# Performance work log

Measured on AMD Instinct MI355X. Metric: run time of the kernel, lower is better.

Reference implementation:

```python
import jax, jax.numpy as jnp
import numpy as np

N = 256      # max_num_nodes (padded nodes per graph)
H = 8        # attention heads
F = 128      # feature_dim
L = 9        # n_layers
INFLA = 6.0  # MCL inflation
EPS = 1e-6


def _layernorm(x, g, b):
    mu = x.mean(-1, keepdims=True)
    var = ((x - mu) ** 2).mean(-1, keepdims=True)
    return (x - mu) / jnp.sqrt(var + 1e-5) * g + b


def _get_mcl(adj):
    # Markov-cluster style power iteration with inflation every 3rd step (num=6)
    m = adj / (adj.sum(-1, keepdims=True) + EPS)
    r = m
    for i in range(6):
        r = m @ r
        if (i + 1) % 3 == 0:
            r = r ** INFLA
        r = r / (r.sum(-1, keepdims=True) + EPS)
    return r


def _forward(input_x, edge_attr, gcn_lin_w, gcn_root_emb, gcn_edge_w,
             gcn_norm_g, gcn_norm_b, ln_in_g, ln_in_b, ln_ffn_g, ln_ffn_b,
             mcl_w, q_w, k_w, v_w, merge_w, merge_b,
             ffn_w1, ffn_b1, ffn_w2, ffn_b2, final_g, final_b,
             edge_index, n_counts, root):
    BN = input_x.shape[0]
    B = BN // N
    dh = F // H
    row, col = edge_index[0], edge_index[1]

    # --- adjacency / padding masks (built once, as in GC_T.forward) ---
    valid = jnp.arange(N)[None, :] < n_counts[:, None]                    # [B,N]
    eb, es, et = row // N, row % N, col % N
    adj = jnp.zeros((B, N, N), bool).at[eb, es, et].set(True)
    adj = adj | (jnp.eye(N, dtype=bool)[None] & valid[:, :, None])        # self loops on valid nodes
    pad = ~(valid[:, :, None] & valid[:, None, :])
    pad_bias = jnp.where(pad, -1024.0, 0.0)[..., None]                    # [B,N,N,1] (broadcast over H)
    mcl = _get_mcl(adj.astype(input_x.dtype))[..., None]                  # [B,N,N,1]

    # --- GCN degree normalization (degree of row index, +1) ---
    deg = jnp.zeros((BN,), input_x.dtype).at[row].add(1.0) + 1.0
    dis = deg ** -0.5
    enorm = (dis[row] * dis[col])[:, None]                                # [E,1]

    out = input_x.reshape(B, N, F)
    for i in range(L):
        # ---- GCNConv: gather-relu-scatter message passing ----
        res = out
        h = out.reshape(BN, F) @ gcn_lin_w[i].T                           # [BN,F]
        ee = edge_attr @ gcn_edge_w[i].T                                  # [E,F]
        msg = enorm * jax.nn.relu(h[row] + ee)                            # x_j = x[row]
        agg = jax.ops.segment_sum(msg, col, num_segments=BN)              # aggregate at target
        g = agg + jax.nn.relu(h + gcn_root_emb[i][root]) / deg[:, None]
        g = jax.nn.relu(_layernorm(g, gcn_norm_g[i], gcn_norm_b[i]))
        out = g.reshape(B, N, F) + res

        # ---- Encoder: biased multi-head attention + FFN ----
        bias4 = (pad_bias + mcl * mcl_w[i][:, 0]).transpose(0, 3, 1, 2)   # [B,H,N,N]
        x = out
        q = (x @ q_w[i].T).reshape(B, N, H, dh).transpose(0, 2, 1, 3) * (dh ** -0.5)
        k = (x @ k_w[i].T).reshape(B, N, H, dh).transpose(0, 2, 1, 3)
        v = (x @ v_w[i].T).reshape(B, N, H, dh).transpose(0, 2, 1, 3)
        att = jax.nn.softmax(jnp.einsum('bhnd,bhmd->bhnm', q, k) + bias4, axis=-1)
        o = jnp.einsum('bhnm,bhmd->bhnd', att, v).transpose(0, 2, 1, 3).reshape(B, N, F)
        o = o @ merge_w[i].T + merge_b[i]
        x = _layernorm(o + x, ln_in_g[i], ln_in_b[i])
        f = jax.nn.gelu(x @ ffn_w1[i].T + ffn_b1[i], approximate=False)
        f = f @ ffn_w2[i].T + ffn_b2[i]
        out = _layernorm(x + f, ln_ffn_g[i], ln_ffn_b[i])

    return _layernorm(out, final_g, final_b)


def setup_inputs() -> dict:
    key = jax.random.key(0)
    ks = jax.random.split(key, 16)
    B, E = 16, 65536
    s = 0.02 * L ** -0.5
    w = lambda k, shape: jax.random.normal(k, shape, jnp.float32) * s
    return {
        'input_x': jax.random.normal(ks[0], (B * N, F), jnp.float32),
        'edge_attr': jax.random.normal(ks[1], (E, 7), jnp.float32),
        'gcn_lin_w': w(ks[2], (L, F, F)),
        'gcn_root_emb': jax.random.normal(ks[3], (L, 2, F), jnp.float32) * 0.02,
        'gcn_edge_w': w(ks[4], (L, F, 7)),
        'gcn_norm_g': jnp.ones((L, F), jnp.float32),
        'gcn_norm_b': jnp.zeros((L, F), jnp.float32),
        'ln_in_g': jnp.ones((L, F), jnp.float32),
        'ln_in_b': jnp.zeros((L, F), jnp.float32),
        'ln_ffn_g': jnp.ones((L, F), jnp.float32),
        'ln_ffn_b': jnp.zeros((L, F), jnp.float32),
        'mcl_w': w(ks[5], (L, H, 1)),
        'q_w': w(ks[6], (L, F, F)),
        'k_w': w(ks[7], (L, F, F)),
        'v_w': w(ks[8], (L, F, F)),
        'merge_w': w(ks[9], (L, F, F)),
        'merge_b': jnp.zeros((L, F), jnp.float32),
        'ffn_w1': w(ks[10], (L, 2 * F, F)),
        'ffn_b1': jnp.zeros((L, 2 * F), jnp.float32),
        'ffn_w2': w(ks[11], (L, F, 2 * F)),
        'ffn_b2': jnp.zeros((L, F), jnp.float32),
        'final_g': jnp.ones((F,), jnp.float32),
        'final_b': jnp.zeros((F,), jnp.float32),
        'edge_index': jax.random.randint(ks[12], (2, E), 0, B * N),
        'n_counts': jax.random.randint(ks[13], (B,), 1, N + 1),
        'root': jax.random.randint(ks[14], (B * N,), 0, 2),
    }


def reference(input_x, edge_attr, gcn_lin_w, gcn_root_emb, gcn_edge_w,
              gcn_norm_g, gcn_norm_b, ln_in_g, ln_in_b, ln_ffn_g, ln_ffn_b,
              mcl_w, q_w, k_w, v_w, merge_w, merge_b,
              ffn_w1, ffn_b1, ffn_w2, ffn_b2, final_g, final_b,
              edge_index, n_counts, root):
    return _forward(input_x, edge_attr, gcn_lin_w, gcn_root_emb, gcn_edge_w,
                    gcn_norm_g, gcn_norm_b, ln_in_g, ln_in_b, ln_ffn_g, ln_ffn_b,
                    mcl_w, q_w, k_w, v_w, merge_w, merge_b,
                    ffn_w1, ffn_b1, ffn_w2, ffn_b2, final_g, final_b,
                    edge_index, n_counts, root)
```

## Files before the change

kernel.cpp:

```cpp
#include <hip/hip_runtime.h>
#include <hip/hip_bf16.h>
#include <math.h>

#define NLAYER 9

typedef unsigned short u16;
typedef __attribute__((ext_vector_type(8))) short short8;
typedef __attribute__((ext_vector_type(4))) float f32x4;

__device__ inline u16 f2bf(float x) {
  unsigned int u = __float_as_uint(x);
  unsigned int r = (u + 0x7fffu + ((u >> 16) & 1u)) >> 16;
  return (u16)r;
}
__device__ inline float gelu_exact(float x) {
  return 0.5f * x * (1.0f + erff(x * 0.7071067811865476f));
}

__global__ void setup1_kernel(const int* __restrict__ ei, float* __restrict__ adj,
                              float* __restrict__ deg, int* __restrict__ ccount, int E, int EB,
                              const float* __restrict__ s0, const float* __restrict__ s1,
                              const float* __restrict__ s2, const float* __restrict__ s3,
                              const float* __restrict__ s4, const float* __restrict__ s5,
                              const float* __restrict__ s6, u16* __restrict__ d0,
                              u16* __restrict__ d1, u16* __restrict__ d2,
                              u16* __restrict__ d3, u16* __restrict__ d4,
                              u16* __restrict__ d5, u16* __restrict__ d6) {
  int bid = blockIdx.x;
  if (bid < EB) {
    int e = bid * 256 + threadIdx.x;
    if (e >= E) return;
    int r = ei[e], c = ei[E + e];
    int b = r >> 8;
    adj[((size_t)b << 16) + ((size_t)(r & 255) << 8) + (c & 255)] = 1.0f;
    atomicAdd(&deg[r], 1.0f);
    atomicAdd(&ccount[c], 1);
  } else {
    int idx = bid - EB;
    int f = idx / 72, cb = idx % 72;
    const float* s;
    u16* d;
    int n;
    switch (f) {
      case 0: s = s0; d = d0; n = NLAYER * 4096; break;
      case 1: s = s1; d = d1; n = NLAYER * 4096; break;
      case 2: s = s2; d = d2; n = NLAYER * 4096; break;
      case 3: s = s3; d = d3; n = NLAYER * 4096; break;
      case 4: s = s4; d = d4; n = NLAYER * 4096; break;
      case 5: s = s5; d = d5; n = NLAYER * 8192; break;
      default: s = s6; d = d6; n = NLAYER * 8192; break;
    }
    for (int i = cb * 256 + threadIdx.x; i < n; i += 72 * 256) {
      float4 v = ((const float4*)s)[i];
      u16 p4[4] = {f2bf(v.x), f2bf(v.y), f2bf(v.z), f2bf(v.w)};
      ((ushort4*)d)[i] = *(ushort4*)p4;
    }
  }
}

__global__ __launch_bounds__(1024) void setup2_kernel(const int* __restrict__ nc,
                                                      float* __restrict__ adj,
                                                      float* __restrict__ deg,
                                                      float* __restrict__ dis,
                                                      const int* __restrict__ ccount,
                                                      int* __restrict__ rowptr, int BN) {
  int bid = blockIdx.x;
  int t = threadIdx.x;
  if (bid < (BN >> 10)) {
    int n = bid * 1024 + t;
    int b = n >> 8, i = n & 255;
    if (i < nc[b]) adj[((size_t)b << 16) + ((size_t)i << 8) + i] = 1.0f;
    float d = deg[n] + 1.0f;
    deg[n] = d;
    dis[n] = rsqrtf(d);
  } else {
    __shared__ int part[1024];
    int base = t * 4;
    int c[4], s = 0;
#pragma unroll
    for (int i = 0; i < 4; i++) { c[i] = (base + i < BN) ? ccount[base + i] : 0; s += c[i]; }
    part[t] = s;
    __syncthreads();
    for (int o = 1; o < 1024; o <<= 1) {
      int v = (t >= o) ? part[t - o] : 0;
      __syncthreads();
      part[t] += v;
      __syncthreads();
    }
    int excl = part[t] - s;
#pragma unroll
    for (int i = 0; i < 4; i++) {
      if (base + i < BN) rowptr[base + i] = excl;
      excl += c[i];
    }
    if (t == 1023) rowptr[BN] = part[1023];
  }
}

__global__ __launch_bounds__(256) void setup3_kernel(const float* __restrict__ m,
                                                     float* __restrict__ rsinv,
                                                     const int* __restrict__ ei,
                                                     const float* __restrict__ dis,
                                                     const int* __restrict__ rowptr,
                                                     int* __restrict__ fill,
                                                     int* __restrict__ src_s,
                                                     int* __restrict__ eidx_s,
                                                     float* __restrict__ enorm_s, int E,
                                                     int BN) {
  int bid = blockIdx.x;
  int w = threadIdx.x >> 6, lane = threadIdx.x & 63;
  if (bid < (BN >> 2)) {
    int row = bid * 4 + w;
    float4 v4 = *(const float4*)(m + (size_t)row * 256 + lane * 4);
    float s = v4.x + v4.y + v4.z + v4.w;
#pragma unroll
    for (int o = 32; o > 0; o >>= 1) s += __shfl_xor(s, o, 64);
    if (lane == 0) rsinv[row] = 1.f / (s + 1e-6f);
  } else {
    int e = (bid - (BN >> 2)) * 256 + threadIdx.x;
    if (e >= E) return;
    int r = ei[e], c = ei[E + e];
    int pos = rowptr[c] + atomicAdd(&fill[c], 1);
    src_s[pos] = r;
    eidx_s[pos] = e;
    enorm_s[pos] = dis[r] * dis[c];
  }
}

__global__ __launch_bounds__(256) void mcl_prep_kernel(const float* __restrict__ m,
                                                       const float* __restrict__ rsinv,
                                                       u16* __restrict__ mb,
                                                       u16* __restrict__ rT) {
  int b = blockIdx.z;
  const float* M = m + ((size_t)b << 16);
  u16* MB = mb + ((size_t)b << 16);
  u16* RT = rT + ((size_t)b << 16);
  int r0 = blockIdx.x * 64, c0 = blockIdx.y * 64;
  __shared__ float ts[64][65];
  int t = threadIdx.x;
  int i = t >> 2, jb = (t & 3) * 16;
  float riv = rsinv[(b << 8) + r0 + i];
#pragma unroll
  for (int g = 0; g < 4; g++) {
    int j = jb + g * 4;
    float4 v = *(const float4*)(M + (size_t)(r0 + i) * 256 + c0 + j);
    v.x *= riv; v.y *= riv; v.z *= riv; v.w *= riv;
    ts[i][j] = v.x; ts[i][j + 1] = v.y; ts[i][j + 2] = v.z; ts[i][j + 3] = v.w;
    u16 p4[4] = {f2bf(v.x), f2bf(v.y), f2bf(v.z), f2bf(v.w)};
    *(ushort4*)(MB + (size_t)(r0 + i) * 256 + c0 + j) = *(ushort4*)p4;
  }
  __syncthreads();
#pragma unroll
  for (int g = 0; g < 4; g++) {
    int j = jb + g * 4;
    u16 p4[4] = {f2bf(ts[j][i]), f2bf(ts[j + 1][i]), f2bf(ts[j + 2][i]), f2bf(ts[j + 3][i])};
    *(ushort4*)(RT + (size_t)(c0 + i) * 256 + r0 + j) = *(ushort4*)p4;
  }
}

__global__ __launch_bounds__(256) void mcl_iter_kernel(const u16* __restrict__ rT,
                                                       const u16* __restrict__ mb,
                                                       u16* __restrict__ rTn,
                                                       float* __restrict__ mclr,
                                                       int inflate, int fin) {
  __shared__ float red[64];
  int b = blockIdx.x >> 4, i0 = (blockIdx.x & 15) * 16;
  int w = threadIdx.x >> 6, lane = threadIdx.x & 63;
  int m16 = lane & 15, quad = lane >> 4;
  const u16* A = rT + ((size_t)b << 16);
  const u16* Bm = mb + ((size_t)b << 16);
  f32x4 acc[4];
#pragma unroll
  for (int tj = 0; tj < 4; tj++) acc[tj] = (f32x4){0.f, 0.f, 0.f, 0.f};
  for (int k0 = 0; k0 < 256; k0 += 32) {
    short8 bb = *(const short8*)(Bm + (size_t)(i0 + m16) * 256 + k0 + quad * 8);
#pragma unroll
    for (int tj = 0; tj < 4; tj++) {
      short8 a = *(const short8*)(A + (size_t)(w * 64 + tj * 16 + m16) * 256 + k0 + quad * 8);
      acc[tj] = __builtin_amdgcn_mfma_f32_16x16x32_bf16(a, bb, acc[tj], 0, 0, 0);
    }
  }
  float ps = 0.f;
#pragma unroll
  for (int tj = 0; tj < 4; tj++)
#pragma unroll
    for (int reg = 0; reg < 4; reg++) {
      float v = acc[tj][reg];
      if (inflate) { float v2 = v * v; v = v2 * v2 * v2; }
      acc[tj][reg] = v;
      ps += v;
    }
  ps += __shfl_xor(ps, 16, 64);
  ps += __shfl_xor(ps, 32, 64);
  if (quad == 0) red[w * 16 + m16] = ps;
  __syncthreads();
  float tot = red[m16] + red[16 + m16] + red[32 + m16] + red[48 + m16];
  float inv = 1.f / (tot + 1e-6f);
  if (fin) {
    float* dst = mclr + ((size_t)b << 16);
#pragma unroll
    for (int tj = 0; tj < 4; tj++)
#pragma unroll
      for (int reg = 0; reg < 4; reg++) {
        int j = w * 64 + tj * 16 + quad * 4 + reg;
        dst[(size_t)(i0 + m16) * 256 + j] = acc[tj][reg] * inv;
      }
  } else {
    u16* dst = rTn + ((size_t)b << 16);
#pragma unroll
    for (int tj = 0; tj < 4; tj++)
#pragma unroll
      for (int reg = 0; reg < 4; reg++) {
        int j = w * 64 + tj * 16 + quad * 4 + reg;
        dst[(size_t)j * 256 + i0 + m16] = f2bf(acc[tj][reg] * inv);
      }
  }
}

__global__ __launch_bounds__(256) void copyx_lin_kernel(const float* __restrict__ x,
                                                        const u16* __restrict__ wlin0,
                                                        float* __restrict__ outb,
                                                        float* __restrict__ hbuf) {
  __shared__ u16 st[16 * 136];
  int m0 = blockIdx.x * 16;
  int tid = threadIdx.x;
  int w = tid >> 6, lane = tid & 63;
  int m16 = lane & 15, quad = lane >> 4;
  for (int i = tid; i < 2048; i += 256) {
    int row = i >> 7, col = i & 127;
    float v = x[(size_t)(m0 + row) * 128 + col];
    outb[(size_t)(m0 + row) * 128 + col] = v;
    st[row * 136 + col] = f2bf(v);
  }
  __syncthreads();
  int c0 = w * 32;
  f32x4 acc[2] = {{0.f, 0.f, 0.f, 0.f}, {0.f, 0.f, 0.f, 0.f}};
#pragma unroll
  for (int k0 = 0; k0 < 128; k0 += 32) {
    short8 a = *(const short8*)(st + m16 * 136 + k0 + quad * 8);
#pragma unroll
    for (int t = 0; t < 2; t++) {
      short8 bb = *(const short8*)(wlin0 + (size_t)(c0 + t * 16 + m16) * 128 + k0 + quad * 8);
      acc[t] = __builtin_amdgcn_mfma_f32_16x16x32_bf16(a, bb, acc[t], 0, 0, 0);
    }
  }
#pragma unroll
  for (int t = 0; t < 2; t++)
#pragma unroll
    for (int reg = 0; reg < 4; reg++)
      hbuf[(size_t)(m0 + quad * 4 + reg) * 128 + c0 + t * 16 + m16] = acc[t][reg];
}

__global__ __launch_bounds__(256) void gcn_ln_kernel(
    const int* __restrict__ rowptr, const int* __restrict__ src_s,
    const int* __restrict__ eidx_s, const float* __restrict__ enorm_s,
    const float* __restrict__ ea, const float* __restrict__ We, const float* __restrict__ h,
    const float* __restrict__ remb, const int* __restrict__ root,
    const float* __restrict__ deg, const float* __restrict__ gamma,
    const float* __restrict__ beta, float* __restrict__ out, u16* __restrict__ out16) {
  __shared__ float Wt[7 * 128];
  __shared__ float part[2][2][128];
  for (int idx = threadIdx.x; idx < 896; idx += 256) {
    int f = idx & 127, k = idx >> 7;
    Wt[k * 128 + f] = We[f * 7 + k];
  }
  __syncthreads();
  int w = threadIdx.x >> 6, lane = threadIdx.x & 63;
  int nodeSlot = w >> 1, wv = w & 1;
  int n = blockIdx.x * 2 + nodeSlot;
  int f0 = lane, f1 = lane + 64;
  int p0 = rowptr[n], p1 = rowptr[n + 1];
  float a0 = 0.f, a1 = 0.f;
  int p = p0 + wv;
  int r = 0, e = 0;
  float en = 0.f, h0 = 0.f, h1 = 0.f;
  if (p < p1) {
    r = src_s[p];
    e = eidx_s[p];
    en = enorm_s[p];
    h0 = h[(size_t)r * 128 + f0];
    h1 = h[(size_t)r * 128 + f1];
  }
  for (; p < p1; p += 2) {
    int enx = 0;
    float ennx = 0.f, hn0 = 0.f, hn1 = 0.f;
    if (p + 2 < p1) {
      int rn = src_s[p + 2];
      enx = eidx_s[p + 2];
      ennx = enorm_s[p + 2];
      hn0 = h[(size_t)rn * 128 + f0];
      hn1 = h[(size_t)rn * 128 + f1];
    }
    const float* eae = ea + (size_t)e * 7;
    float d0 = 0.f, d1 = 0.f;
#pragma unroll
    for (int k = 0; k < 7; k++) {
      float ev = eae[k];
      d0 += ev * Wt[k * 128 + f0];
      d1 += ev * Wt[k * 128 + f1];
    }
    a0 += en * fmaxf(h0 + d0, 0.f);
    a1 += en * fmaxf(h1 + d1, 0.f);
    e = enx;
    en = ennx;
    h0 = hn0;
    h1 = hn1;
  }
  part[nodeSlot][wv][lane] = a0;
  part[nodeSlot][wv][64 + lane] = a1;
  __syncthreads();
  if (wv == 0) {
    a0 = part[nodeSlot][0][lane] + part[nodeSlot][1][lane];
    a1 = part[nodeSlot][0][64 + lane] + part[nodeSlot][1][64 + lane];
    float invd = 1.0f / deg[n];
    const float* re = remb + root[n] * 128;
    size_t base = (size_t)n * 128;
    float g0 = a0 + fmaxf(h[base + f0] + re[f0], 0.f) * invd;
    float g1 = a1 + fmaxf(h[base + f1] + re[f1], 0.f) * invd;
    float s = g0 + g1, ss = g0 * g0 + g1 * g1;
#pragma unroll
    for (int o = 32; o > 0; o >>= 1) {
      s += __shfl_xor(s, o, 64);
      ss += __shfl_xor(ss, o, 64);
    }
    float mu = s * 0.0078125f;
    float var = ss * 0.0078125f - mu * mu;
    float rs = rsqrtf(var + 1e-5f);
    float y0 = fmaxf((g0 - mu) * rs * gamma[f0] + beta[f0], 0.f) + out[base + f0];
    float y1 = fmaxf((g1 - mu) * rs * gamma[f1] + beta[f1], 0.f) + out[base + f1];
    out[base + f0] = y0;
    out[base + f1] = y1;
    out16[base + f0] = f2bf(y0);
    out16[base + f1] = f2bf(y1);
  }
}

__global__ __launch_bounds__(256) void attn_qkv_kernel(
    const u16* __restrict__ x16, const u16* __restrict__ wq, const u16* __restrict__ wk,
    const u16* __restrict__ wv, const float* __restrict__ mclr,
    const float* __restrict__ mclw, const int* __restrict__ ncnt, u16* __restrict__ o) {
  __shared__ float ks[256][16];
  __shared__ float vs[256][16];
  __shared__ float qs[64][16];
  int qt = blockIdx.x, hh = blockIdx.y, b = blockIdx.z;
  int t = threadIdx.x;
  int w = t >> 6, lane = t & 63;
  int m16 = lane & 15, quad = lane >> 4;
  const u16* bk = wk + (size_t)(hh * 16 + m16) * 128 + quad * 8;
  const u16* bv = wv + (size_t)(hh * 16 + m16) * 128 + quad * 8;
#pragma unroll
  for (int tj = 0; tj < 4; tj++) {
    int rb = w * 64 + tj * 16;
    const u16* arow = x16 + (size_t)(b * 256 + rb + m16) * 128 + quad * 8;
    f32x4 ak = {0.f, 0.f, 0.f, 0.f}, av = {0.f, 0.f, 0.f, 0.f};
#pragma unroll
    for (int k0 = 0; k0 < 128; k0 += 32) {
      short8 a = *(const short8*)(arow + k0);
      ak = __builtin_amdgcn_mfma_f32_16x16x32_bf16(a, *(const short8*)(bk + k0), ak, 0, 0, 0);
      av = __builtin_amdgcn_mfma_f32_16x16x32_bf16(a, *(const short8*)(bv + k0), av, 0, 0, 0);
    }
#pragma unroll
    for (int reg = 0; reg < 4; reg++) {
      ks[rb + quad * 4 + reg][m16] = ak[reg];
      vs[rb + quad * 4 + reg][m16] = av[reg];
    }
  }
  {
    const u16* bq = wq + (size_t)(hh * 16 + m16) * 128 + quad * 8;
    const u16* arow = x16 + (size_t)(b * 256 + qt * 64 + w * 16 + m16) * 128 + quad * 8;
    f32x4 aq = {0.f, 0.f, 0.f, 0.f};
#pragma unroll
    for (int k0 = 0; k0 < 128; k0 += 32) {
      short8 a = *(const short8*)(arow + k0);
      aq = __builtin_amdgcn_mfma_f32_16x16x32_bf16(a, *(const short8*)(bq + k0), aq, 0, 0, 0);
    }
#pragma unroll
    for (int reg = 0; reg < 4; reg++) qs[w * 16 + quad * 4 + reg][m16] = aq[reg] * 0.25f;
  }
  __syncthreads();
  int i = qt * 64 + (t >> 2);
  int d0 = (t & 3) * 4;
  int nc = ncnt[b];
  bool vi = i < nc;
  float wh = mclw[hh];
  float qv[4] = {qs[t >> 2][d0], qs[t >> 2][d0 + 1], qs[t >> 2][d0 + 2], qs[t >> 2][d0 + 3]};
  const float* mrow = mclr + ((size_t)(b * 256 + i)) * 256;
  float acc[4] = {0.f, 0.f, 0.f, 0.f};
  float lsum = 0.f;
  for (int j0 = 0; j0 < 256; j0 += 4) {
    float4 mc = *(const float4*)(mrow + j0);
    float mcv[4] = {mc.x, mc.y, mc.z, mc.w};
#pragma unroll
    for (int jj = 0; jj < 4; jj++) {
      int j = j0 + jj;
      float s = qv[0] * ks[j][d0] + qv[1] * ks[j][d0 + 1] + qv[2] * ks[j][d0 + 2] +
                qv[3] * ks[j][d0 + 3];
      s += __shfl_xor(s, 1, 64);
      s += __shfl_xor(s, 2, 64);
      float bias = mcv[jj] * wh + ((vi && j >= nc) ? -1024.f : 0.f);
      float pe = __expf(s + bias);
      lsum += pe;
      acc[0] += pe * vs[j][d0];
      acc[1] += pe * vs[j][d0 + 1];
      acc[2] += pe * vs[j][d0 + 2];
      acc[3] += pe * vs[j][d0 + 3];
    }
  }
  float inv = 1.f / lsum;
  u16 p4[4] = {f2bf(acc[0] * inv), f2bf(acc[1] * inv), f2bf(acc[2] * inv), f2bf(acc[3] * inv)};
  *(ushort4*)(o + ((size_t)(b * 256 + i) * 128 + hh * 16 + d0)) = *(ushort4*)p4;
}

__global__ __launch_bounds__(256) void merge_ffn_kernel(
    const u16* __restrict__ ob16, const u16* __restrict__ Wm, const float* __restrict__ mb,
    const float* __restrict__ gam1, const float* __restrict__ bet1,
    const u16* __restrict__ W1, const float* __restrict__ b1, const u16* __restrict__ W2,
    const float* __restrict__ b2, const float* __restrict__ gam2,
    const float* __restrict__ bet2, float* __restrict__ outb,
    const u16* __restrict__ wlin_next, float* __restrict__ hbuf,
    const float* __restrict__ fing, const float* __restrict__ finb) {
  __shared__ float redS[64], redSS[64];
  __shared__ u16 st[16 * 136];
  __shared__ u16 f1s[16 * 264];
  int tid = threadIdx.x;
  int w = tid >> 6, lane = tid & 63;
  int m16 = lane & 15, quad = lane >> 4;
  int m0 = blockIdx.x * 16;
  f32x4 acc[2] = {{0.f, 0.f, 0.f, 0.f}, {0.f, 0.f, 0.f, 0.f}};
  {
    const u16* arow = ob16 + (size_t)(m0 + m16) * 128 + quad * 8;
#pragma unroll
    for (int k0 = 0; k0 < 128; k0 += 32) {
      short8 a = *(const short8*)(arow + k0);
#pragma unroll
      for (int t = 0; t < 2; t++) {
        short8 bb = *(const short8*)(Wm + (size_t)(w * 32 + t * 16 + m16) * 128 + k0 + quad * 8);
        acc[t] = __builtin_amdgcn_mfma_f32_16x16x32_bf16(a, bb, acc[t], 0, 0, 0);
      }
    }
  }
  float s4[4] = {0.f, 0.f, 0.f, 0.f}, ss4[4] = {0.f, 0.f, 0.f, 0.f};
#pragma unroll
  for (int t = 0; t < 2; t++) {
    int col = w * 32 + t * 16 + m16;
    float bi = mb[col];
#pragma unroll
    for (int reg = 0; reg < 4; reg++) {
      int row = m0 + quad * 4 + reg;
      float v = acc[t][reg] + bi + outb[(size_t)row * 128 + col];
      acc[t][reg] = v;
      s4[reg] += v;
      ss4[reg] += v * v;
    }
  }
#pragma unroll
  for (int o = 1; o <= 8; o <<= 1)
#pragma unroll
    for (int reg = 0; reg < 4; reg++) {
      s4[reg] += __shfl_xor(s4[reg], o, 64);
      ss4[reg] += __shfl_xor(ss4[reg], o, 64);
    }
  if (m16 == 0) {
#pragma unroll
    for (int reg = 0; reg < 4; reg++) {
      redS[w * 16 + quad * 4 + reg] = s4[reg];
      redSS[w * 16 + quad * 4 + reg] = ss4[reg];
    }
  }
  __syncthreads();
  float mu[4], rsd[4];
#pragma unroll
  for (int reg = 0; reg < 4; reg++) {
    int r = quad * 4 + reg;
    float S = redS[r] + redS[16 + r] + redS[32 + r] + redS[48 + r];
    float SS = redSS[r] + redSS[16 + r] + redSS[32 + r] + redSS[48 + r];
    mu[reg] = S * 0.0078125f;
    float var = SS * 0.0078125f - mu[reg] * mu[reg];
    rsd[reg] = rsqrtf(var + 1e-5f);
  }
  float xr[2][4];
#pragma unroll
  for (int t = 0; t < 2; t++) {
    int col = w * 32 + t * 16 + m16;
    float g = gam1[col], be = bet1[col];
#pragma unroll
    for (int reg = 0; reg < 4; reg++) {
      float y = (acc[t][reg] - mu[reg]) * rsd[reg] * g + be;
      xr[t][reg] = y;
      st[(quad * 4 + reg) * 136 + col] = f2bf(y);
    }
  }
  __syncthreads();
  {
    f32x4 acc1[4];
#pragma unroll
    for (int t = 0; t < 4; t++) acc1[t] = (f32x4){0.f, 0.f, 0.f, 0.f};
#pragma unroll
    for (int k0 = 0; k0 < 128; k0 += 32) {
      short8 a = *(const short8*)(st + m16 * 136 + k0 + quad * 8);
#pragma unroll
      for (int t = 0; t < 4; t++) {
        short8 bb = *(const short8*)(W1 + (size_t)(w * 64 + t * 16 + m16) * 128 + k0 + quad * 8);
        acc1[t] = __builtin_amdgcn_mfma_f32_16x16x32_bf16(a, bb, acc1[t], 0, 0, 0);
      }
    }
#pragma unroll
    for (int t = 0; t < 4; t++) {
      int col = w * 64 + t * 16 + m16;
      float bi = b1[col];
#pragma unroll
      for (int reg = 0; reg < 4; reg++)
        f1s[(quad * 4 + reg) * 264 + col] = f2bf(gelu_exact(acc1[t][reg] + bi));
    }
  }
  __syncthreads();
#pragma unroll
  for (int t = 0; t < 2; t++) acc[t] = (f32x4){0.f, 0.f, 0.f, 0.f};
#pragma unroll
  for (int k0 = 0; k0 < 256; k0 += 32) {
    short8 a = *(const short8*)(f1s + m16 * 264 + k0 + quad * 8);
#pragma unroll
    for (int t = 0; t < 2; t++) {
      short8 bb = *(const short8*)(W2 + (size_t)(w * 32 + t * 16 + m16) * 256 + k0 + quad * 8);
      acc[t] = __builtin_amdgcn_mfma_f32_16x16x32_bf16(a, bb, acc[t], 0, 0, 0);
    }
  }
#pragma unroll
  for (int reg = 0; reg < 4; reg++) { s4[reg] = 0.f; ss4[reg] = 0.f; }
#pragma unroll
  for (int t = 0; t < 2; t++) {
    int col = w * 32 + t * 16 + m16;
    float bi = b2[col];
#pragma unroll
    for (int reg = 0; reg < 4; reg++) {
      float v = acc[t][reg] + bi + xr[t][reg];
      acc[t][reg] = v;
      s4[reg] += v;
      ss4[reg] += v * v;
    }
  }
#pragma unroll
  for (int o = 1; o <= 8; o <<= 1)
#pragma unroll
    for (int reg = 0; reg < 4; reg++) {
      s4[reg] += __shfl_xor(s4[reg], o, 64);
      ss4[reg] += __shfl_xor(ss4[reg], o, 64);
    }
  __syncthreads();
  if (m16 == 0) {
#pragma unroll
    for (int reg = 0; reg < 4; reg++) {
      redS[w * 16 + quad * 4 + reg] = s4[reg];
      redSS[w * 16 + quad * 4 + reg] = ss4[reg];
    }
  }
  __syncthreads();
#pragma unroll
  for (int reg = 0; reg < 4; reg++) {
    int r = quad * 4 + reg;
    float S = redS[r] + redS[16 + r] + redS[32 + r] + redS[48 + r];
    float SS = redSS[r] + redSS[16 + r] + redSS[32 + r] + redSS[48 + r];
    mu[reg] = S * 0.0078125f;
    float var = SS * 0.0078125f - mu[reg] * mu[reg];
    rsd[reg] = rsqrtf(var + 1e-5f);
  }
#pragma unroll
  for (int t = 0; t < 2; t++) {
    int col = w * 32 + t * 16 + m16;
    float g = gam2[col], be = bet2[col];
#pragma unroll
    for (int reg = 0; reg < 4; reg++)
      acc[t][reg] = (acc[t][reg] - mu[reg]) * rsd[reg] * g + be;
  }
  if (fing) {
    float s2[4] = {0.f, 0.f, 0.f, 0.f}, ss2[4] = {0.f, 0.f, 0.f, 0.f};
#pragma unroll
    for (int t = 0; t < 2; t++)
#pragma unroll
      for (int reg = 0; reg < 4; reg++) {
        float v = acc[t][reg];
        s2[reg] += v;
        ss2[reg] += v * v;
      }
#pragma unroll
    for (int o = 1; o <= 8; o <<= 1)
#pragma unroll
      for (int reg = 0; reg < 4; reg++) {
        s2[reg] += __shfl_xor(s2[reg], o, 64);
        ss2[reg] += __shfl_xor(ss2[reg], o, 64);
      }
    __syncthreads();
    if (m16 == 0) {
#pragma unroll
      for (int reg = 0; reg < 4; reg++) {
        redS[w * 16 + quad * 4 + reg] = s2[reg];
        redSS[w * 16 + quad * 4 + reg] = ss2[reg];
      }
    }
    __syncthreads();
#pragma unroll
    for (int reg = 0; reg < 4; reg++) {
      int r = quad * 4 + reg;
      float S = redS[r] + redS[16 + r] + redS[32 + r] + redS[48 + r];
      float SS = redSS[r] + redSS[16 + r] + redSS[32 + r] + redSS[48 + r];
      mu[reg] = S * 0.0078125f;
      float var = SS * 0.0078125f - mu[reg] * mu[reg];
      rsd[reg] = rsqrtf(var + 1e-5f);
    }
#pragma unroll
    for (int t = 0; t < 2; t++) {
      int col = w * 32 + t * 16 + m16;
      float g = fing[col], be = finb[col];
#pragma unroll
      for (int reg = 0; reg < 4; reg++) {
        int row = m0 + quad * 4 + reg;
        outb[(size_t)row * 128 + col] = (acc[t][reg] - mu[reg]) * rsd[reg] * g + be;
      }
    }
    return;
  }
#pragma unroll
  for (int t = 0; t < 2; t++) {
    int col = w * 32 + t * 16 + m16;
#pragma unroll
    for (int reg = 0; reg < 4; reg++) {
      int row = m0 + quad * 4 + reg;
      float y = acc[t][reg];
      outb[(size_t)row * 128 + col] = y;
      st[(quad * 4 + reg) * 136 + col] = f2bf(y);
    }
  }
  __syncthreads();
  {
    f32x4 acc2[2] = {{0.f, 0.f, 0.f, 0.f}, {0.f, 0.f, 0.f, 0.f}};
#pragma unroll
    for (int k0 = 0; k0 < 128; k0 += 32) {
      short8 a = *(const short8*)(st + m16 * 136 + k0 + quad * 8);
#pragma unroll
      for (int t = 0; t < 2; t++) {
        short8 bb =
            *(const short8*)(wlin_next + (size_t)(w * 32 + t * 16 + m16) * 128 + k0 + quad * 8);
        acc2[t] = __builtin_amdgcn_mfma_f32_16x16x32_bf16(a, bb, acc2[t], 0, 0, 0);
      }
    }
#pragma unroll
    for (int t = 0; t < 2; t++)
#pragma unroll
      for (int reg = 0; reg < 4; reg++)
        hbuf[(size_t)(m0 + quad * 4 + reg) * 128 + w * 32 + t * 16 + m16] = acc2[t][reg];
  }
}

extern "C" void kernel_launch(void* const* d_in, const int* in_sizes, int n_in,
                              void* d_out, int out_size, void* d_ws, size_t ws_size,
                              hipStream_t stream) {
  const float* input_x = (const float*)d_in[0];
  const float* edge_attr = (const float*)d_in[1];
  const float* gcn_lin_w = (const float*)d_in[2];
  const float* gcn_root = (const float*)d_in[3];
  const float* gcn_edge_w = (const float*)d_in[4];
  const float* gcn_ng = (const float*)d_in[5];
  const float* gcn_nb = (const float*)d_in[6];
  const float* ln_in_g = (const float*)d_in[7];
  const float* ln_in_b = (const float*)d_in[8];
  const float* ln_ffn_g = (const float*)d_in[9];
  const float* ln_ffn_b = (const float*)d_in[10];
  const float* mcl_w = (const float*)d_in[11];
  const float* q_w = (const float*)d_in[12];
  const float* k_w = (const float*)d_in[13];
  const float* v_w = (const float*)d_in[14];
  const float* merge_w = (const float*)d_in[15];
  const float* merge_b = (const float*)d_in[16];
  const float* ffn_w1 = (const float*)d_in[17];
  const float* ffn_b1 = (const float*)d_in[18];
  const float* ffn_w2 = (const float*)d_in[19];
  const float* ffn_b2 = (const float*)d_in[20];
  const float* final_g = (const float*)d_in[21];
  const float* final_b = (const float*)d_in[22];
  const int* edge_index = (const int*)d_in[23];
  const int* n_counts = (const int*)d_in[24];
  const int* root = (const int*)d_in[25];

  const int E = in_sizes[23] / 2;
  const int B = in_sizes[24];
  const int BN = B * 256;
  const int EB = (E + 255) / 256;

  float* ws = (float*)d_ws;
  size_t off = 0;
  auto alloc = [&](size_t n) {
    off = (off + 3) & ~(size_t)3;
    float* q = ws + off;
    off += n;
    return q;
  };
  const size_t NN2 = (size_t)B * 256 * 256;
  const size_t XF = (size_t)BN * 128;
  float* mclr = alloc(NN2);
  float* mbuf = alloc(NN2);
  float* hbuf = alloc(XF);
  float* deg = alloc(BN);
  int* ccount = (int*)alloc(BN);
  int* fill = (int*)alloc(BN);
  float* dis = alloc(BN);
  float* rsinv = alloc(BN);
  int* rowptr = (int*)alloc(BN + 1);
  int* src_s = (int*)alloc(E);
  int* eidx_s = (int*)alloc(E);
  float* enorm_s = alloc(E);
  u16* mb16 = (u16*)alloc(NN2 / 2);
  u16* rT16 = (u16*)alloc(NN2 / 2);
  u16* cT16 = (u16*)alloc(NN2 / 2);
  u16* ob16 = (u16*)alloc(XF / 2);
  u16* outb16 = (u16*)alloc(XF / 2);
  u16* wlin16 = (u16*)alloc((size_t)NLAYER * 8192);
  u16* wq16 = (u16*)alloc((size_t)NLAYER * 8192);
  u16* wk16 = (u16*)alloc((size_t)NLAYER * 8192);
  u16* wv16 = (u16*)alloc((size_t)NLAYER * 8192);
  u16* wm16 = (u16*)alloc((size_t)NLAYER * 8192);
  u16* wf116 = (u16*)alloc((size_t)NLAYER * 16384);
  u16* wf216 = (u16*)alloc((size_t)NLAYER * 16384);
  float* outb = (float*)d_out;

  hipMemsetAsync(mbuf, 0, NN2 * sizeof(float), stream);
  hipMemsetAsync(deg, 0, 3 * BN * sizeof(float), stream);
  setup1_kernel<<<EB + 504, 256, 0, stream>>>(edge_index, mbuf, deg, ccount, E, EB, gcn_lin_w,
                                              q_w, k_w, v_w, merge_w, ffn_w1, ffn_w2, wlin16,
                                              wq16, wk16, wv16, wm16, wf116, wf216);
  setup2_kernel<<<BN / 1024 + 1, 1024, 0, stream>>>(n_counts, mbuf, deg, dis, ccount, rowptr,
                                                    BN);
  setup3_kernel<<<BN / 4 + EB, 256, 0, stream>>>(mbuf, rsinv, edge_index, dis, rowptr, fill,
                                                 src_s, eidx_s, enorm_s, E, BN);
  dim3 mmg(4, 4, B);
  mcl_prep_kernel<<<mmg, 256, 0, stream>>>(mbuf, rsinv, mb16, rT16);
  {
    u16 *cur = rT16, *nxt = cT16;
    for (int it = 0; it < 6; it++) {
      int inflate = (it == 2 || it == 5) ? 1 : 0;
      mcl_iter_kernel<<<16 * B, 256, 0, stream>>>(cur, mb16, nxt, mclr, inflate,
                                                  it == 5 ? 1 : 0);
      u16* tmp = cur;
      cur = nxt;
      nxt = tmp;
    }
  }
  copyx_lin_kernel<<<BN / 16, 256, 0, stream>>>(input_x, wlin16, outb, hbuf);

  dim3 ag(4, 8, B);
  for (int l = 0; l < NLAYER; l++) {
    gcn_ln_kernel<<<BN / 2, 256, 0, stream>>>(
        rowptr, src_s, eidx_s, enorm_s, edge_attr, gcn_edge_w + (size_t)l * 896, hbuf,
        gcn_root + (size_t)l * 256, root, deg, gcn_ng + l * 128, gcn_nb + l * 128, outb,
        outb16);
    attn_qkv_kernel<<<ag, 256, 0, stream>>>(outb16, wq16 + (size_t)l * 16384,
                                            wk16 + (size_t)l * 16384,
                                            wv16 + (size_t)l * 16384, mclr, mcl_w + l * 8,
                                            n_counts, ob16);
    const u16* wnext = (l + 1 < NLAYER) ? (wlin16 + (size_t)(l + 1) * 16384) : wlin16;
    const float* fg = (l == NLAYER - 1) ? final_g : nullptr;
    const float* fb = (l == NLAYER - 1) ? final_b : nullptr;
    merge_ffn_kernel<<<BN / 16, 256, 0, stream>>>(
        ob16, wm16 + (size_t)l * 16384, merge_b + l * 128, ln_in_g + l * 128,
        ln_in_b + l * 128, wf116 + (size_t)l * 32768, ffn_b1 + l * 256,
        wf216 + (size_t)l * 32768, ffn_b2 + l * 128, ln_ffn_g + l * 128, ln_ffn_b + l * 128,
        outb, wnext, hbuf, fg, fb);
  }
}
```

Baseline: 762.5 us.

## Build adjacency directly in bf16 and fold input copy/linear into setup kernel

The dense adjacency is now stored as bf16 in the existing mb16 buffer instead of a separate fp32 buffer, which halves the memset and adjacency traffic and lets mcl_prep normalize in place. The separate copyx_lin kernel is merged into setup2 as extra 1024-thread blocks handling 64 rows each, removing one launch. The attention loop is unrolled to 8 keys per iteration and the padding test is simplified to a single precomputed threshold. Risk: the merged blocks run with 1024 threads and a larger shared-memory footprint, which may lower occupancy for that part.

```diff
diff --git a/kernel.cpp b/kernel.cpp
--- a/kernel.cpp
+++ b/kernel.cpp
@@ -13,11 +13,14 @@
   unsigned int r = (u + 0x7fffu + ((u >> 16) & 1u)) >> 16;
   return (u16)r;
 }
+__device__ inline float bf2f(u16 s) { return __uint_as_float(((unsigned int)s) << 16); }
 __device__ inline float gelu_exact(float x) {
   return 0.5f * x * (1.0f + erff(x * 0.7071067811865476f));
 }
 
-__global__ void setup1_kernel(const int* __restrict__ ei, float* __restrict__ adj,
+#define BF16_ONE 0x3F80u
+
+__global__ void setup1_kernel(const int* __restrict__ ei, u16* __restrict__ adjb,
                               float* __restrict__ deg, int* __restrict__ ccount, int E, int EB,
                               const float* __restrict__ s0, const float* __restrict__ s1,
                               const float* __restrict__ s2, const float* __restrict__ s3,
@@ -32,7 +35,7 @@
     if (e >= E) return;
     int r = ei[e], c = ei[E + e];
     int b = r >> 8;
-    adj[((size_t)b << 16) + ((size_t)(r & 255) << 8) + (c & 255)] = 1.0f;
+    adjb[((size_t)b << 16) + ((size_t)(r & 255) << 8) + (c & 255)] = (u16)BF16_ONE;
     atomicAdd(&deg[r], 1.0f);
     atomicAdd(&ccount[c], 1);
   } else {
@@ -58,23 +61,24 @@
   }
 }
 
-__global__ __launch_bounds__(1024) void setup2_kernel(const int* __restrict__ nc,
-                                                      float* __restrict__ adj,
-                                                      float* __restrict__ deg,
-                                                      float* __restrict__ dis,
-                                                      const int* __restrict__ ccount,
-                                                      int* __restrict__ rowptr, int BN) {
+__global__ __launch_bounds__(1024) void setup2_kernel(
+    const int* __restrict__ nc, u16* __restrict__ adjb, float* __restrict__ deg,
+    float* __restrict__ dis, const int* __restrict__ ccount, int* __restrict__ rowptr, int BN,
+    const float* __restrict__ x, const u16* __restrict__ wlin0, float* __restrict__ outb,
+    float* __restrict__ hbuf) {
+  __shared__ u16 smem_u[64 * 136];
   int bid = blockIdx.x;
   int t = threadIdx.x;
-  if (bid < (BN >> 10)) {
+  int NSL = BN >> 10;
+  if (bid < NSL) {
     int n = bid * 1024 + t;
     int b = n >> 8, i = n & 255;
-    if (i < nc[b]) adj[((size_t)b << 16) + ((size_t)i << 8) + i] = 1.0f;
+    if (i < nc[b]) adjb[((size_t)b << 16) + ((size_t)i << 8) + i] = (u16)BF16_ONE;
     float d = deg[n] + 1.0f;
     deg[n] = d;
     dis[n] = rsqrtf(d);
-  } else {
-    __shared__ int part[1024];
+  } else if (bid == NSL) {
+    int* part = (int*)smem_u;
     int base = t * 4;
     int c[4], s = 0;
 #pragma unroll
@@ -94,10 +98,40 @@
       excl += c[i];
     }
     if (t == 1023) rowptr[BN] = part[1023];
-  }
-}
-
-__global__ __launch_bounds__(256) void setup3_kernel(const float* __restrict__ m,
+  } else {
+    int m0 = (bid - NSL - 1) * 64;
+    for (int i = t; i < 8192; i += 1024) {
+      int row = i >> 7, col = i & 127;
+      float v = x[(size_t)(m0 + row) * 128 + col];
+      outb[(size_t)(m0 + row) * 128 + col] = v;
+      smem_u[row * 136 + col] = f2bf(v);
+    }
+    __syncthreads();
+    int w = t >> 6, lane = t & 63;
+    int m16 = lane & 15, quad = lane >> 4;
+    int rowg = w >> 2, colg = w & 3;
+    int c0 = colg * 32;
+    f32x4 acc[2] = {{0.f, 0.f, 0.f, 0.f}, {0.f, 0.f, 0.f, 0.f}};
+#pragma unroll
+    for (int k0 = 0; k0 < 128; k0 += 32) {
+      short8 a = *(const short8*)(smem_u + (rowg * 16 + m16) * 136 + k0 + quad * 8);
+#pragma unroll
+      for (int tt = 0; tt < 2; tt++) {
+        short8 bb =
+            *(const short8*)(wlin0 + (size_t)(c0 + tt * 16 + m16) * 128 + k0 + quad * 8);
+        acc[tt] = __builtin_amdgcn_mfma_f32_16x16x32_bf16(a, bb, acc[tt], 0, 0, 0);
+      }
+    }
+#pragma unroll
+    for (int tt = 0; tt < 2; tt++)
+#pragma unroll
+      for (int reg = 0; reg < 4; reg++)
+        hbuf[(size_t)(m0 + rowg * 16 + quad * 4 + reg) * 128 + c0 + tt * 16 + m16] =
+            acc[tt][reg];
+  }
+}
+
+__global__ __launch_bounds__(256) void setup3_kernel(const u16* __restrict__ adjb,
                                                      float* __restrict__ rsinv,
                                                      const int* __restrict__ ei,
                                                      const float* __restrict__ dis,
@@ -111,8 +145,8 @@
   int w = threadIdx.x >> 6, lane = threadIdx.x & 63;
   if (bid < (BN >> 2)) {
     int row = bid * 4 + w;
-    float4 v4 = *(const float4*)(m + (size_t)row * 256 + lane * 4);
-    float s = v4.x + v4.y + v4.z + v4.w;
+    ushort4 v4 = *(const ushort4*)(adjb + (size_t)row * 256 + lane * 4);
+    float s = bf2f(v4.x) + bf2f(v4.y) + bf2f(v4.z) + bf2f(v4.w);
 #pragma unroll
     for (int o = 32; o > 0; o >>= 1) s += __shfl_xor(s, o, 64);
     if (lane == 0) rsinv[row] = 1.f / (s + 1e-6f);
@@ -127,12 +161,10 @@
   }
 }
 
-__global__ __launch_bounds__(256) void mcl_prep_kernel(const float* __restrict__ m,
+__global__ __launch_bounds__(256) void mcl_prep_kernel(u16* __restrict__ mb,
                                                        const float* __restrict__ rsinv,
-                                                       u16* __restrict__ mb,
                                                        u16* __restrict__ rT) {
   int b = blockIdx.z;
-  const float* M = m + ((size_t)b << 16);
   u16* MB = mb + ((size_t)b << 16);
   u16* RT = rT + ((size_t)b << 16);
   int r0 = blockIdx.x * 64, c0 = blockIdx.y * 64;
@@ -143,10 +175,11 @@
 #pragma unroll
   for (int g = 0; g < 4; g++) {
     int j = jb + g * 4;
-    float4 v = *(const float4*)(M + (size_t)(r0 + i) * 256 + c0 + j);
-    v.x *= riv; v.y *= riv; v.z *= riv; v.w *= riv;
-    ts[i][j] = v.x; ts[i][j + 1] = v.y; ts[i][j + 2] = v.z; ts[i][j + 3] = v.w;
-    u16 p4[4] = {f2bf(v.x), f2bf(v.y), f2bf(v.z), f2bf(v.w)};
+    ushort4 u4 = *(const ushort4*)(MB + (size_t)(r0 + i) * 256 + c0 + j);
+    float vx = bf2f(u4.x) * riv, vy = bf2f(u4.y) * riv, vz = bf2f(u4.z) * riv,
+          vw = bf2f(u4.w) * riv;
+    ts[i][j] = vx; ts[i][j + 1] = vy; ts[i][j + 2] = vz; ts[i][j + 3] = vw;
+    u16 p4[4] = {f2bf(vx), f2bf(vy), f2bf(vz), f2bf(vw)};
     *(ushort4*)(MB + (size_t)(r0 + i) * 256 + c0 + j) = *(ushort4*)p4;
   }
   __syncthreads();
@@ -215,40 +248,6 @@
         dst[(size_t)j * 256 + i0 + m16] = f2bf(acc[tj][reg] * inv);
       }
   }
-}
-
-__global__ __launch_bounds__(256) void copyx_lin_kernel(const float* __restrict__ x,
-                                                        const u16* __restrict__ wlin0,
-                                                        float* __restrict__ outb,
-                                                        float* __restrict__ hbuf) {
-  __shared__ u16 st[16 * 136];
-  int m0 = blockIdx.x * 16;
-  int tid = threadIdx.x;
-  int w = tid >> 6, lane = tid & 63;
-  int m16 = lane & 15, quad = lane >> 4;
-  for (int i = tid; i < 2048; i += 256) {
-    int row = i >> 7, col = i & 127;
-    float v = x[(size_t)(m0 + row) * 128 + col];
-    outb[(size_t)(m0 + row) * 128 + col] = v;
-    st[row * 136 + col] = f2bf(v);
-  }
-  __syncthreads();
-  int c0 = w * 32;
-  f32x4 acc[2] = {{0.f, 0.f, 0.f, 0.f}, {0.f, 0.f, 0.f, 0.f}};
-#pragma unroll
-  for (int k0 = 0; k0 < 128; k0 += 32) {
-    short8 a = *(const short8*)(st + m16 * 136 + k0 + quad * 8);
-#pragma unroll
-    for (int t = 0; t < 2; t++) {
-      short8 bb = *(const short8*)(wlin0 + (size_t)(c0 + t * 16 + m16) * 128 + k0 + quad * 8);
-      acc[t] = __builtin_amdgcn_mfma_f32_16x16x32_bf16(a, bb, acc[t], 0, 0, 0);
-    }
-  }
-#pragma unroll
-  for (int t = 0; t < 2; t++)
-#pragma unroll
-    for (int reg = 0; reg < 4; reg++)
-      hbuf[(size_t)(m0 + quad * 4 + reg) * 128 + c0 + t * 16 + m16] = acc[t][reg];
 }
 
 __global__ __launch_bounds__(256) void gcn_ln_kernel(
@@ -382,22 +381,24 @@
   int d0 = (t & 3) * 4;
   int nc = ncnt[b];
   bool vi = i < nc;
+  int jpad = vi ? nc : 257;
   float wh = mclw[hh];
   float qv[4] = {qs[t >> 2][d0], qs[t >> 2][d0 + 1], qs[t >> 2][d0 + 2], qs[t >> 2][d0 + 3]};
   const float* mrow = mclr + ((size_t)(b * 256 + i)) * 256;
   float acc[4] = {0.f, 0.f, 0.f, 0.f};
   float lsum = 0.f;
-  for (int j0 = 0; j0 < 256; j0 += 4) {
-    float4 mc = *(const float4*)(mrow + j0);
-    float mcv[4] = {mc.x, mc.y, mc.z, mc.w};
-#pragma unroll
-    for (int jj = 0; jj < 4; jj++) {
+  for (int j0 = 0; j0 < 256; j0 += 8) {
+    float4 mc0 = *(const float4*)(mrow + j0);
+    float4 mc1 = *(const float4*)(mrow + j0 + 4);
+    float mcv[8] = {mc0.x, mc0.y, mc0.z, mc0.w, mc1.x, mc1.y, mc1.z, mc1.w};
+#pragma unroll
+    for (int jj = 0; jj < 8; jj++) {
       int j = j0 + jj;
       float s = qv[0] * ks[j][d0] + qv[1] * ks[j][d0 + 1] + qv[2] * ks[j][d0 + 2] +
                 qv[3] * ks[j][d0 + 3];
       s += __shfl_xor(s, 1, 64);
       s += __shfl_xor(s, 2, 64);
-      float bias = mcv[jj] * wh + ((vi && j >= nc) ? -1024.f : 0.f);
+      float bias = mcv[jj] * wh + ((j >= jpad) ? -1024.f : 0.f);
       float pe = __expf(s + bias);
       lsum += pe;
       acc[0] += pe * vs[j][d0];
@@ -697,7 +698,6 @@
   const size_t NN2 = (size_t)B * 256 * 256;
   const size_t XF = (size_t)BN * 128;
   float* mclr = alloc(NN2);
-  float* mbuf = alloc(NN2);
   float* hbuf = alloc(XF);
   float* deg = alloc(BN);
   int* ccount = (int*)alloc(BN);
@@ -722,17 +722,17 @@
   u16* wf216 = (u16*)alloc((size_t)NLAYER * 16384);
   float* outb = (float*)d_out;
 
-  hipMemsetAsync(mbuf, 0, NN2 * sizeof(float), stream);
+  hipMemsetAsync(mb16, 0, NN2 * sizeof(u16), stream);
   hipMemsetAsync(deg, 0, 3 * BN * sizeof(float), stream);
-  setup1_kernel<<<EB + 504, 256, 0, stream>>>(edge_index, mbuf, deg, ccount, E, EB, gcn_lin_w,
+  setup1_kernel<<<EB + 504, 256, 0, stream>>>(edge_index, mb16, deg, ccount, E, EB, gcn_lin_w,
                                               q_w, k_w, v_w, merge_w, ffn_w1, ffn_w2, wlin16,
                                               wq16, wk16, wv16, wm16, wf116, wf216);
-  setup2_kernel<<<BN / 1024 + 1, 1024, 0, stream>>>(n_counts, mbuf, deg, dis, ccount, rowptr,
-                                                    BN);
-  setup3_kernel<<<BN / 4 + EB, 256, 0, stream>>>(mbuf, rsinv, edge_index, dis, rowptr, fill,
+  setup2_kernel<<<(BN >> 10) + 1 + (BN >> 6), 1024, 0, stream>>>(
+      n_counts, mb16, deg, dis, ccount, rowptr, BN, input_x, wlin16, outb, hbuf);
+  setup3_kernel<<<BN / 4 + EB, 256, 0, stream>>>(mb16, rsinv, edge_index, dis, rowptr, fill,
                                                  src_s, eidx_s, enorm_s, E, BN);
   dim3 mmg(4, 4, B);
-  mcl_prep_kernel<<<mmg, 256, 0, stream>>>(mbuf, rsinv, mb16, rT16);
+  mcl_prep_kernel<<<mmg, 256, 0, stream>>>(mb16, rsinv, rT16);
   {
     u16 *cur = rT16, *nxt = cT16;
     for (int it = 0; it < 6; it++) {
@@ -744,7 +744,6 @@
       nxt = tmp;
     }
   }
-  copyx_lin_kernel<<<BN / 16, 256, 0, stream>>>(input_x, wlin16, outb, hbuf);
 
   dim3 ag(4, 8, B);
   for (int l = 0; l < NLAYER; l++) {
```

Result: no change. 764.8 us (+0.3%).
